# Kernel tuning notes

Hardware: AMD Instinct MI355X
Metric: run time of the kernel (lower is better)

## Reference

```python
import jax, jax.numpy as jnp
import numpy as np

LEAKY_SLOPE = 0.2  # PyG GATConv default negative_slope
EPS = 1e-16


def _gat_layer(h_in, src, dst, W, a_src, a_dst, b, concat):
    # h_in: [N, Fin]; src/dst: [Etot] (self-loops included); W: [Fin, H*C]
    N = h_in.shape[0]
    H, C = a_src.shape
    h = (h_in @ W).reshape(N, H, C)                       # [N,H,C]
    al_s = jnp.sum(h * a_src, axis=-1)                    # [N,H]
    al_d = jnp.sum(h * a_dst, axis=-1)                    # [N,H]
    e = jax.nn.leaky_relu(al_s[src] + al_d[dst], LEAKY_SLOPE)  # [E,H]
    emax = jax.ops.segment_max(e, dst, num_segments=N)    # segment softmax over dst
    p = jnp.exp(e - emax[dst])
    denom = jax.ops.segment_sum(p, dst, num_segments=N)
    alpha = p / (denom[dst] + EPS)                        # [E,H]
    out = jax.ops.segment_sum(h[src] * alpha[:, :, None], dst, num_segments=N)  # [N,H,C]
    out = out.reshape(N, H * C) if concat else out.mean(axis=1)
    return out + b


def setup_inputs() -> dict:
    key = jax.random.key(0)
    ks = jax.random.split(key, 16)
    N, E, Fin, Hd, Hh = 10000, 320000, 256, 128, 4

    def glorot(k, shape, fan_in):
        return jax.random.normal(k, shape, dtype=jnp.float32) * (1.0 / np.sqrt(fan_in))

    inp = {
        "x": jax.random.normal(ks[0], (N, Fin), dtype=jnp.float32),
        "edge_index": jax.random.randint(ks[1], (2, E), 0, N, dtype=jnp.int32),
        # conv1: Fin -> Hd x Hh heads, concat
        "W1": glorot(ks[2], (Fin, Hh * Hd), Fin),
        "a1_src": glorot(ks[3], (Hh, Hd), Hd),
        "a1_dst": glorot(ks[4], (Hh, Hd), Hd),
        "b1": jnp.zeros((Hh * Hd,), jnp.float32),
        # conv2: Hh*Hd -> Hd x Hh heads, concat
        "W2": glorot(ks[5], (Hh * Hd, Hh * Hd), Hh * Hd),
        "a2_src": glorot(ks[6], (Hh, Hd), Hd),
        "a2_dst": glorot(ks[7], (Hh, Hd), Hd),
        "b2": jnp.zeros((Hh * Hd,), jnp.float32),
        # conv3: Hh*Hd -> Hd, 1 head, concat=False (mean)
        "W3": glorot(ks[8], (Hh * Hd, Hd), Hh * Hd),
        "a3_src": glorot(ks[9], (1, Hd), Hd),
        "a3_dst": glorot(ks[10], (1, Hd), Hd),
        "b3": jnp.zeros((Hd,), jnp.float32),
        # classifier: Hd -> Hd//2 -> 2
        "Wc1": glorot(ks[11], (Hd, Hd // 2), Hd),
        "bc1": jnp.zeros((Hd // 2,), jnp.float32),
        "Wc2": glorot(ks[12], (Hd // 2, 2), Hd // 2),
        "bc2": jnp.zeros((2,), jnp.float32),
    }
    return inp


def reference(x, edge_index, W1, a1_src, a1_dst, b1, W2, a2_src, a2_dst, b2,
              W3, a3_src, a3_dst, b3, Wc1, bc1, Wc2, bc2):
    N = x.shape[0]
    loops = jnp.arange(N, dtype=edge_index.dtype)
    src = jnp.concatenate([edge_index[0], loops])  # PyG adds self-loops
    dst = jnp.concatenate([edge_index[1], loops])

    h = jax.nn.elu(_gat_layer(x, src, dst, W1, a1_src, a1_dst, b1, concat=True))
    h = jax.nn.elu(_gat_layer(h, src, dst, W2, a2_src, a2_dst, b2, concat=True))
    embeddings = _gat_layer(h, src, dst, W3, a3_src, a3_dst, b3, concat=False)  # [N, 128]
    out = jax.nn.relu(embeddings @ Wc1 + bc1) @ Wc2 + bc2  # [N, 2]
    return out, embeddings
```

## Files before the change

### kernel.cpp

```cpp
#include <hip/hip_runtime.h>
#include <cstddef>

#define LEAKY 0.2f
#define EPS_DEN 1e-16f

typedef short bf8_t __attribute__((ext_vector_type(8)));
typedef float f4_t __attribute__((ext_vector_type(4)));
typedef unsigned short us4_t __attribute__((ext_vector_type(4)));

__device__ __forceinline__ unsigned short f2bf(float f) {
    unsigned u = __float_as_uint(f);
    unsigned r = (u + 0x7fffu + ((u >> 16) & 1u)) >> 16;
    return (unsigned short)r;
}
__device__ __forceinline__ float bf2f(unsigned short h) {
    return __uint_as_float(((unsigned)h) << 16);
}

__global__ void hist_kernel(const int* __restrict__ dst, int* __restrict__ counts, int E) {
    int i = blockIdx.x * blockDim.x + threadIdx.x;
    if (i < E) atomicAdd(&counts[dst[i]], 1);
}

__global__ void scan1_kernel(int* __restrict__ cnt, int* __restrict__ bsum, int N) {
    __shared__ int s[256];
    int t = threadIdx.x;
    int i = blockIdx.x * 256 + t;
    int v = (i < N) ? cnt[i] : 0;
    s[t] = v;
    __syncthreads();
#pragma unroll
    for (int st = 1; st < 256; st <<= 1) {
        int add = (t >= st) ? s[t - st] : 0;
        __syncthreads();
        s[t] += add;
        __syncthreads();
    }
    if (i < N) cnt[i] = s[t] - v;
    if (t == 255) bsum[blockIdx.x] = s[255];
}

__global__ void scan3b_kernel(int* __restrict__ cnt, const int* __restrict__ bsum,
                              int* __restrict__ offs, int N, int NB) {
    __shared__ int sPre[64];
    __shared__ int sTot;
    int t = threadIdx.x;
    if (t < 64) {
        int v = (t < NB) ? bsum[t] : 0;
        int inc = v;
#pragma unroll
        for (int off = 1; off < 64; off <<= 1) {
            int u = __shfl_up(inc, off);
            if (t >= off) inc += u;
        }
        sPre[t] = inc - v;
        if (t == 63) sTot = inc;
    }
    __syncthreads();
    int i = blockIdx.x * 256 + t;
    if (i < N) {
        int o = cnt[i] + sPre[blockIdx.x];
        offs[i] = o;
        cnt[i] = o;
    }
    if (blockIdx.x == 0 && t == 0) offs[N] = sTot;
}

__global__ void scatter_kernel(const int* __restrict__ src, const int* __restrict__ dst,
                               int* __restrict__ cursor, int* __restrict__ csrc, int E) {
    int i = blockIdx.x * blockDim.x + threadIdx.x;
    if (i < E) {
        int d = dst[i];
        int pos = atomicAdd(&cursor[d], 1);
        csrc[pos] = src[i];
    }
}

__global__ void split_all_kernel(
    const float* __restrict__ x, unsigned short* __restrict__ xh, unsigned short* __restrict__ xl,
    int NBX,
    const float* __restrict__ W1, unsigned short* __restrict__ w1h, unsigned short* __restrict__ w1l,
    const float* __restrict__ W2, unsigned short* __restrict__ w2h, unsigned short* __restrict__ w2l,
    const float* __restrict__ W3, unsigned short* __restrict__ w3h, unsigned short* __restrict__ w3l) {
    int b = blockIdx.x, t = threadIdx.x;
    float v;
    unsigned short* ph;
    unsigned short* pl;
    int out;
    if (b < NBX) {
        int idx = b * 256 + t;
        v = x[idx];
        out = idx;
        ph = xh; pl = xl;
    } else if (b < NBX + 512) {
        int idx = (b - NBX) * 256 + t;
        v = W1[idx];
        int k = idx >> 9, n = idx & 511;
        out = n * 256 + k;
        ph = w1h; pl = w1l;
    } else if (b < NBX + 512 + 1024) {
        int idx = (b - NBX - 512) * 256 + t;
        v = W2[idx];
        int k = idx >> 9, n = idx & 511;
        out = n * 512 + k;
        ph = w2h; pl = w2l;
    } else {
        int idx = (b - NBX - 1536) * 256 + t;
        v = W3[idx];
        int k = idx >> 7, n = idx & 127;
        out = n * 512 + k;
        ph = w3h; pl = w3l;
    }
    unsigned short hv = f2bf(v);
    ph[out] = hv;
    pl[out] = f2bf(v - bf2f(hv));
}

__global__ __launch_bounds__(256) void mfma_gemm128_kernel(
    const unsigned short* __restrict__ Ahi, const unsigned short* __restrict__ Alo,
    const unsigned short* __restrict__ BThi, const unsigned short* __restrict__ BTlo,
    const float* __restrict__ a_src, const float* __restrict__ a_dst,
    float* __restrict__ C, float* __restrict__ als, float* __restrict__ ald,
    int M, int N, int K) {
    constexpr int BK = 64;
    __shared__ __align__(16) unsigned short sAh[128 * BK];
    __shared__ __align__(16) unsigned short sAl[128 * BK];
    __shared__ __align__(16) unsigned short sBh[128 * BK];
    __shared__ __align__(16) unsigned short sBl[128 * BK];
    __shared__ float sAls[128][2];
    __shared__ float sAld[128][2];
    int t = threadIdx.x;
    int w = t >> 6, lane = t & 63;
    int quad = lane >> 4, low = lane & 15;
    int m0 = blockIdx.y * 128, n0 = blockIdx.x * 128;
    int wm = (w & 1) * 64, wn = (w >> 1) * 64;

    f4_t acc[4][4];
#pragma unroll
    for (int i = 0; i < 4; i++)
#pragma unroll
        for (int j = 0; j < 4; j++) acc[i][j] = (f4_t){0.f, 0.f, 0.f, 0.f};

    int srow = lane >> 3;
    int schunk = lane & 7;

    for (int k0 = 0; k0 < K; k0 += BK) {
        __syncthreads();
#pragma unroll
        for (int inst = 0; inst < 4; inst++) {
            int rl = w * 32 + inst * 8 + srow;
            int gm = m0 + rl;
            if (gm >= M) gm = M - 1;
            size_t goff = (size_t)gm * K + k0 + schunk * 8;
            size_t loff = (size_t)rl * 128 - (size_t)(lane * 16) + (size_t)(srow * 128 + schunk * 16);
            loff = (size_t)(w * 32 + inst * 8) * 128;
            __builtin_amdgcn_global_load_lds(
                (const __attribute__((address_space(1))) void*)(Ahi + goff),
                (__attribute__((address_space(3))) void*)((char*)sAh + loff), 16, 0, 0);
            __builtin_amdgcn_global_load_lds(
                (const __attribute__((address_space(1))) void*)(Alo + goff),
                (__attribute__((address_space(3))) void*)((char*)sAl + loff), 16, 0, 0);
        }
#pragma unroll
        for (int inst = 0; inst < 4; inst++) {
            int rl = w * 32 + inst * 8 + srow;
            int gn = n0 + rl;
            size_t goff = (size_t)gn * K + k0 + schunk * 8;
            size_t loff = (size_t)(w * 32 + inst * 8) * 128;
            __builtin_amdgcn_global_load_lds(
                (const __attribute__((address_space(1))) void*)(BThi + goff),
                (__attribute__((address_space(3))) void*)((char*)sBh + loff), 16, 0, 0);
            __builtin_amdgcn_global_load_lds(
                (const __attribute__((address_space(1))) void*)(BTlo + goff),
                (__attribute__((address_space(3))) void*)((char*)sBl + loff), 16, 0, 0);
        }
        __syncthreads();

#pragma unroll
        for (int ks = 0; ks < 2; ks++) {
            int ko = ks * 32 + quad * 8;
            bf8_t afh[4], bfh[4], xx[4];
#pragma unroll
            for (int i = 0; i < 4; i++) {
                int row = wm + i * 16 + low;
                afh[i] = *(const bf8_t*)&sAh[row * BK + ko];
            }
#pragma unroll
            for (int j = 0; j < 4; j++) {
                int row = wn + j * 16 + low;
                bfh[j] = *(const bf8_t*)&sBh[row * BK + ko];
            }
#pragma unroll
            for (int i = 0; i < 4; i++)
#pragma unroll
                for (int j = 0; j < 4; j++)
                    acc[i][j] = __builtin_amdgcn_mfma_f32_16x16x32_bf16(afh[i], bfh[j], acc[i][j], 0, 0, 0);
#pragma unroll
            for (int j = 0; j < 4; j++) {
                int row = wn + j * 16 + low;
                xx[j] = *(const bf8_t*)&sBl[row * BK + ko];
            }
#pragma unroll
            for (int i = 0; i < 4; i++)
#pragma unroll
                for (int j = 0; j < 4; j++)
                    acc[i][j] = __builtin_amdgcn_mfma_f32_16x16x32_bf16(afh[i], xx[j], acc[i][j], 0, 0, 0);
#pragma unroll
            for (int i = 0; i < 4; i++) {
                int row = wm + i * 16 + low;
                xx[i] = *(const bf8_t*)&sAl[row * BK + ko];
            }
#pragma unroll
            for (int i = 0; i < 4; i++)
#pragma unroll
                for (int j = 0; j < 4; j++)
                    acc[i][j] = __builtin_amdgcn_mfma_f32_16x16x32_bf16(xx[i], bfh[j], acc[i][j], 0, 0, 0);
        }
    }

#pragma unroll
    for (int i = 0; i < 4; i++) {
#pragma unroll
        for (int r = 0; r < 4; r++) {
            int gm = m0 + wm + i * 16 + quad * 4 + r;
            if (gm >= M) continue;
#pragma unroll
            for (int j = 0; j < 4; j++) {
                int gn = n0 + wn + j * 16 + low;
                C[(size_t)gm * N + gn] = acc[i][j][r];
            }
        }
    }

    int hd = n0 >> 7;
    float as_[4], ad_[4];
#pragma unroll
    for (int j = 0; j < 4; j++) {
        int c = wn + j * 16 + low;
        as_[j] = a_src[hd * 128 + c];
        ad_[j] = a_dst[hd * 128 + c];
    }
    int chh = wn >> 6;
#pragma unroll
    for (int i = 0; i < 4; i++) {
#pragma unroll
        for (int r = 0; r < 4; r++) {
            float v = acc[i][0][r] * as_[0] + acc[i][1][r] * as_[1] +
                      acc[i][2][r] * as_[2] + acc[i][3][r] * as_[3];
            float vd = acc[i][0][r] * ad_[0] + acc[i][1][r] * ad_[1] +
                       acc[i][2][r] * ad_[2] + acc[i][3][r] * ad_[3];
#pragma unroll
            for (int off = 1; off < 16; off <<= 1) {
                v += __shfl_xor(v, off);
                vd += __shfl_xor(vd, off);
            }
            if (low == 0) {
                int row = wm + i * 16 + quad * 4 + r;
                sAls[row][chh] = v;
                sAld[row][chh] = vd;
            }
        }
    }
    __syncthreads();
    if (t < 128) {
        int gm = m0 + t;
        if (gm < M) {
            als[gm * 4 + hd] = sAls[t][0] + sAls[t][1];
            ald[gm * 4 + hd] = sAld[t][0] + sAld[t][1];
        }
    }
}

__global__ __launch_bounds__(256) void mfma_gemm64_kernel(
    const unsigned short* __restrict__ Ahi, const unsigned short* __restrict__ Alo,
    const unsigned short* __restrict__ BThi, const unsigned short* __restrict__ BTlo,
    const float* __restrict__ a_src, const float* __restrict__ a_dst,
    float* __restrict__ C, float* __restrict__ als, float* __restrict__ ald,
    int M, int N, int K) {
    constexpr int BK = 32;
    __shared__ __align__(16) unsigned short sAh[64 * BK];
    __shared__ __align__(16) unsigned short sAl[64 * BK];
    __shared__ __align__(16) unsigned short sBh[128 * BK];
    __shared__ __align__(16) unsigned short sBl[128 * BK];
    __shared__ float sAls[64][2];
    __shared__ float sAld[64][2];
    int t = threadIdx.x;
    int w = t >> 6, lane = t & 63;
    int quad = lane >> 4, low = lane & 15;
    int m0 = blockIdx.y * 64, n0 = blockIdx.x * 128;
    int wm = (w & 1) * 32, wn = (w >> 1) * 64;

    f4_t acc[2][4];
#pragma unroll
    for (int i = 0; i < 2; i++)
#pragma unroll
        for (int j = 0; j < 4; j++) acc[i][j] = (f4_t){0.f, 0.f, 0.f, 0.f};

    int srow = lane >> 2;
    int schunk = lane & 3;

    for (int k0 = 0; k0 < K; k0 += BK) {
        __syncthreads();
        {
            int gm = m0 + w * 16 + srow;
            if (gm >= M) gm = M - 1;
            size_t goff = (size_t)gm * K + k0 + schunk * 8;
            size_t loff = (size_t)(w * 1024);
            __builtin_amdgcn_global_load_lds(
                (const __attribute__((address_space(1))) void*)(Ahi + goff),
                (__attribute__((address_space(3))) void*)((char*)sAh + loff), 16, 0, 0);
            __builtin_amdgcn_global_load_lds(
                (const __attribute__((address_space(1))) void*)(Alo + goff),
                (__attribute__((address_space(3))) void*)((char*)sAl + loff), 16, 0, 0);
        }
#pragma unroll
        for (int inst = 0; inst < 2; inst++) {
            int gn = n0 + w * 32 + inst * 16 + srow;
            size_t goff = (size_t)gn * K + k0 + schunk * 8;
            size_t loff = (size_t)(w * 2048 + inst * 1024);
            __builtin_amdgcn_global_load_lds(
                (const __attribute__((address_space(1))) void*)(BThi + goff),
                (__attribute__((address_space(3))) void*)((char*)sBh + loff), 16, 0, 0);
            __builtin_amdgcn_global_load_lds(
                (const __attribute__((address_space(1))) void*)(BTlo + goff),
                (__attribute__((address_space(3))) void*)((char*)sBl + loff), 16, 0, 0);
        }
        __syncthreads();

        bf8_t afh[2], bfh[4], xx[4];
#pragma unroll
        for (int i = 0; i < 2; i++) {
            int row = wm + i * 16 + low;
            afh[i] = *(const bf8_t*)&sAh[row * BK + quad * 8];
        }
#pragma unroll
        for (int j = 0; j < 4; j++) {
            int row = wn + j * 16 + low;
            bfh[j] = *(const bf8_t*)&sBh[row * BK + quad * 8];
        }
#pragma unroll
        for (int i = 0; i < 2; i++)
#pragma unroll
            for (int j = 0; j < 4; j++)
                acc[i][j] = __builtin_amdgcn_mfma_f32_16x16x32_bf16(afh[i], bfh[j], acc[i][j], 0, 0, 0);
#pragma unroll
        for (int j = 0; j < 4; j++) {
            int row = wn + j * 16 + low;
            xx[j] = *(const bf8_t*)&sBl[row * BK + quad * 8];
        }
#pragma unroll
        for (int i = 0; i < 2; i++)
#pragma unroll
            for (int j = 0; j < 4; j++)
                acc[i][j] = __builtin_amdgcn_mfma_f32_16x16x32_bf16(afh[i], xx[j], acc[i][j], 0, 0, 0);
#pragma unroll
        for (int i = 0; i < 2; i++) {
            int row = wm + i * 16 + low;
            xx[i] = *(const bf8_t*)&sAl[row * BK + quad * 8];
        }
#pragma unroll
        for (int i = 0; i < 2; i++)
#pragma unroll
            for (int j = 0; j < 4; j++)
                acc[i][j] = __builtin_amdgcn_mfma_f32_16x16x32_bf16(xx[i], bfh[j], acc[i][j], 0, 0, 0);
    }

#pragma unroll
    for (int i = 0; i < 2; i++) {
#pragma unroll
        for (int r = 0; r < 4; r++) {
            int gm = m0 + wm + i * 16 + quad * 4 + r;
            if (gm >= M) continue;
#pragma unroll
            for (int j = 0; j < 4; j++) {
                int gn = n0 + wn + j * 16 + low;
                C[(size_t)gm * N + gn] = acc[i][j][r];
            }
        }
    }

    float as_[4], ad_[4];
#pragma unroll
    for (int j = 0; j < 4; j++) {
        int c = wn + j * 16 + low;
        as_[j] = a_src[c];
        ad_[j] = a_dst[c];
    }
    int chh = wn >> 6;
#pragma unroll
    for (int i = 0; i < 2; i++) {
#pragma unroll
        for (int r = 0; r < 4; r++) {
            float v = acc[i][0][r] * as_[0] + acc[i][1][r] * as_[1] +
                      acc[i][2][r] * as_[2] + acc[i][3][r] * as_[3];
            float vd = acc[i][0][r] * ad_[0] + acc[i][1][r] * ad_[1] +
                       acc[i][2][r] * ad_[2] + acc[i][3][r] * ad_[3];
#pragma unroll
            for (int off = 1; off < 16; off <<= 1) {
                v += __shfl_xor(v, off);
                vd += __shfl_xor(vd, off);
            }
            if (low == 0) {
                int row = wm + i * 16 + quad * 4 + r;
                sAls[row][chh] = v;
                sAld[row][chh] = vd;
            }
        }
    }
    __syncthreads();
    if (t < 64) {
        int gm = m0 + t;
        if (gm < M) {
            als[gm] = sAls[t][0] + sAls[t][1];
            ald[gm] = sAld[t][0] + sAld[t][1];
        }
    }
}

__global__ void stats_h4_kernel(const int* __restrict__ csrc, const int* __restrict__ offs,
                                const float* __restrict__ als, const float* __restrict__ ald,
                                float* __restrict__ pbuf, float* __restrict__ psf,
                                float* __restrict__ rden, int N, int E) {
    int wave = threadIdx.x >> 6, lane = threadIdx.x & 63;
    int n = blockIdx.x * 4 + wave;
    if (n >= N) return;
    int hd = lane & 3, es = lane >> 2;
    float aldn = ald[n * 4 + hd];
    float selfe = als[n * 4 + hd] + aldn;
    selfe = selfe > 0.f ? selfe : LEAKY * selfe;
    int beg = offs[n], end = offs[n + 1];
    int deg = end - beg;
    float* pb = pbuf + (size_t)hd * E;
    float m = selfe;
    float d = 0.f;
    if (deg <= 64) {
        float eR[4];
        int nch = (deg + 15) >> 4;
        for (int k = 0; k < nch; k++) {
            int idx = beg + k * 16 + es;
            float e = -1e30f;
            if (idx < end) {
                int s = csrc[idx];
                e = als[s * 4 + hd] + aldn;
                e = e > 0.f ? e : LEAKY * e;
                m = fmaxf(m, e);
            }
            eR[k] = e;
        }
#pragma unroll
        for (int off = 4; off < 64; off <<= 1) m = fmaxf(m, __shfl_xor(m, off));
        for (int k = 0; k < nch; k++) {
            int idx = beg + k * 16 + es;
            if (idx < end) {
                float p = __expf(eR[k] - m);
                pb[idx] = p;
                d += p;
            }
        }
    } else {
        for (int base = beg; base + es < end; base += 16) {
            int idx = base + es;
            int s = csrc[idx];
            float e = als[s * 4 + hd] + aldn;
            e = e > 0.f ? e : LEAKY * e;
            pb[idx] = e;
            m = fmaxf(m, e);
        }
#pragma unroll
        for (int off = 4; off < 64; off <<= 1) m = fmaxf(m, __shfl_xor(m, off));
        for (int base = beg; base + es < end; base += 16) {
            int idx = base + es;
            float p = __expf(pb[idx] - m);
            pb[idx] = p;
            d += p;
        }
    }
#pragma unroll
    for (int off = 4; off < 64; off <<= 1) d += __shfl_xor(d, off);
    float pself = __expf(selfe - m);
    float r = 1.0f / (d + pself + EPS_DEN);
    if (es == 0) {
        psf[n * 4 + hd] = pself;
        rden[n * 4 + hd] = r;
    }
}

template <bool DO_ELU>
__global__ __launch_bounds__(64) void gat_agg_hh_kernel(
    const float* __restrict__ h, const float* __restrict__ pbuf,
    const float* __restrict__ psf, const float* __restrict__ rden,
    const int* __restrict__ csrc, const int* __restrict__ offs,
    const float* __restrict__ bias, unsigned short* __restrict__ ohi,
    unsigned short* __restrict__ olo, int N, int E) {
    int gid = blockIdx.x;
    int hh = gid & 7;
    int n = gid >> 3;
    int head = hh >> 1;
    int lane = threadIdx.x;
    int eg = lane >> 4;
    int f0 = hh * 64 + (lane & 15) * 4;
    const float* pb = pbuf + (size_t)head * E;

    __shared__ int   sSrc[2][64];
    __shared__ float sP[2][64];
    int beg = offs[n], end = offs[n + 1];
    int nchunks = (end - beg + 63) >> 6;

    f4_t acc = (f4_t){0.f, 0.f, 0.f, 0.f};
    if (beg + lane < end) {
        sSrc[0][lane] = csrc[beg + lane] << 9;
        sP[0][lane] = pb[beg + lane];
    }
    for (int ch = 0; ch < nchunks; ch++) {
        int base = beg + ch * 64;
        int len = min(64, end - base);
        int buf = ch & 1;
        __syncthreads();
        int nbase = base + 64;
        if (ch + 1 < nchunks && nbase + lane < end) {
            sSrc[buf ^ 1][lane] = csrc[nbase + lane] << 9;
            sP[buf ^ 1][lane] = pb[nbase + lane];
        }
#pragma unroll 8
        for (int c = eg; c < len; c += 4) {
            const float* srow = h + (size_t)(unsigned)sSrc[buf][c] + f0;
            acc += sP[buf][c] * *(const f4_t*)srow;
        }
    }
    if (eg == 0) {
        f4_t x = *(const f4_t*)(h + (size_t)n * 512 + f0);
        acc += psf[n * 4 + head] * x;
    }
#pragma unroll
    for (int j = 0; j < 4; j++) {
        acc[j] += __shfl_xor(acc[j], 16);
        acc[j] += __shfl_xor(acc[j], 32);
    }
    if (lane < 16) {
        float r = rden[n * 4 + head];
        f4_t b = *(const f4_t*)(bias + f0);
        us4_t hs, ls;
#pragma unroll
        for (int j = 0; j < 4; j++) {
            float o = acc[j] * r + b[j];
            if (DO_ELU) o = o > 0.f ? o : (__expf(o) - 1.0f);
            unsigned short hv = f2bf(o);
            hs[j] = hv;
            ls[j] = f2bf(o - bf2f(hv));
        }
        size_t idx = (size_t)n * 512 + f0;
        *(us4_t*)&ohi[idx] = hs;
        *(us4_t*)&olo[idx] = ls;
    }
}

__global__ __launch_bounds__(256) void gat_agg_h1_cls_kernel(
    const float* __restrict__ h, const float* __restrict__ als,
    const float* __restrict__ ald, const int* __restrict__ csrc,
    const int* __restrict__ offs, const float* __restrict__ bias,
    const float* __restrict__ Wc1, const float* __restrict__ bc1,
    const float* __restrict__ Wc2, const float* __restrict__ bc2,
    float* __restrict__ emb, float* __restrict__ outp, int N) {
    int tid = threadIdx.x;
    int wave = tid >> 6;
    int n = blockIdx.x * 4 + wave;
    int lane = tid & 63;
    int eg = lane >> 4;
    int fl = (lane & 15) * 8;
    __shared__ float sW[128 * 64];
    __shared__ float semb[4][128];

    for (int i = tid; i < 128 * 64; i += 256) sW[i] = Wc1[i];

    int beg = offs[n], end = offs[n + 1];
    int deg = end - beg;
    float aldn = ald[n];
    float selfe = als[n] + aldn;
    selfe = selfe > 0.f ? selfe : LEAKY * selfe;

    f4_t a0 = (f4_t){0.f, 0.f, 0.f, 0.f};
    f4_t a1 = (f4_t){0.f, 0.f, 0.f, 0.f};
    float d = 0.f;
    float m;

    if (deg <= 64) {
        float e = -1e30f;
        int s = 0;
        if (lane < deg) {
            s = csrc[beg + lane];
            e = als[s] + aldn;
            e = e > 0.f ? e : LEAKY * e;
        }
        m = fmaxf(e, selfe);
#pragma unroll
        for (int off = 1; off < 64; off <<= 1) m = fmaxf(m, __shfl_xor(m, off));
        float p = (lane < deg) ? __expf(e - m) : 0.f;
        d = p;
        int sreg = s << 7;
        int maxit = (deg + 3) >> 2;
#pragma unroll 4
        for (int i = 0; i < maxit; i++) {
            int c = eg + i * 4;
            int soff = __shfl(sreg, c);
            float pc = __shfl(p, c);
            const float* srow = h + (size_t)(unsigned)soff + fl;
            a0 += pc * *(const f4_t*)(srow);
            a1 += pc * *(const f4_t*)(srow + 4);
        }
    } else {
        m = selfe;
        for (int i = beg + lane; i < end; i += 64) {
            int s = csrc[i];
            float e = als[s] + aldn;
            e = e > 0.f ? e : LEAKY * e;
            m = fmaxf(m, e);
        }
#pragma unroll
        for (int off = 1; off < 64; off <<= 1) m = fmaxf(m, __shfl_xor(m, off));
        for (int base = beg; base < end; base += 64) {
            int len = min(64, end - base);
            int sreg = 0;
            float p = 0.f;
            if (lane < len) {
                int s = csrc[base + lane];
                float e = als[s] + aldn;
                e = e > 0.f ? e : LEAKY * e;
                p = __expf(e - m);
                sreg = s << 7;
                d += p;
            }
            int maxit = (len + 3) >> 2;
#pragma unroll 4
            for (int i = 0; i < maxit; i++) {
                int c = eg + i * 4;
                int soff = __shfl(sreg, c);
                float pc = __shfl(p, c);
                const float* srow = h + (size_t)(unsigned)soff + fl;
                a0 += pc * *(const f4_t*)(srow);
                a1 += pc * *(const f4_t*)(srow + 4);
            }
        }
    }

    float pself = __expf(selfe - m);
    if (eg == 0) {
        const float* srow = h + (size_t)n * 128 + fl;
        a0 += pself * *(const f4_t*)(srow);
        a1 += pself * *(const f4_t*)(srow + 4);
    }
#pragma unroll
    for (int j = 0; j < 4; j++) {
        a0[j] += __shfl_xor(a0[j], 16);
        a0[j] += __shfl_xor(a0[j], 32);
        a1[j] += __shfl_xor(a1[j], 16);
        a1[j] += __shfl_xor(a1[j], 32);
    }
#pragma unroll
    for (int off = 1; off < 64; off <<= 1) d += __shfl_xor(d, off);
    float r = 1.0f / (d + pself + EPS_DEN);

    if (lane < 16) {
        int fo = lane * 8;
        f4_t b0 = *(const f4_t*)(bias + fo);
        f4_t b1 = *(const f4_t*)(bias + fo + 4);
        f4_t o0, o1;
#pragma unroll
        for (int j = 0; j < 4; j++) {
            o0[j] = a0[j] * r + b0[j];
            o1[j] = a1[j] * r + b1[j];
        }
        *(f4_t*)&semb[wave][fo] = o0;
        *(f4_t*)&semb[wave][fo + 4] = o1;
        *(f4_t*)&emb[(size_t)n * 128 + fo] = o0;
        *(f4_t*)&emb[(size_t)n * 128 + fo + 4] = o1;
    }
    __syncthreads();

    float cacc = bc1[lane];
#pragma unroll 8
    for (int k = 0; k < 128; k++) cacc += semb[wave][k] * sW[k * 64 + lane];
    cacc = fmaxf(cacc, 0.f);
    float o0 = cacc * Wc2[lane * 2 + 0];
    float o1 = cacc * Wc2[lane * 2 + 1];
#pragma unroll
    for (int off = 32; off; off >>= 1) {
        o0 += __shfl_down(o0, off);
        o1 += __shfl_down(o1, off);
    }
    if (lane == 0) {
        outp[n * 2 + 0] = o0 + bc2[0];
        outp[n * 2 + 1] = o1 + bc2[1];
    }
}

extern "C" void kernel_launch(void* const* d_in, const int* in_sizes, int n_in,
                              void* d_out, int out_size, void* d_ws, size_t ws_size,
                              hipStream_t stream) {
    const float* x      = (const float*)d_in[0];
    const int*   ei     = (const int*)d_in[1];
    const float* W1     = (const float*)d_in[2];
    const float* a1s    = (const float*)d_in[3];
    const float* a1d    = (const float*)d_in[4];
    const float* b1     = (const float*)d_in[5];
    const float* W2     = (const float*)d_in[6];
    const float* a2s    = (const float*)d_in[7];
    const float* a2d    = (const float*)d_in[8];
    const float* b2     = (const float*)d_in[9];
    const float* W3     = (const float*)d_in[10];
    const float* a3s    = (const float*)d_in[11];
    const float* a3d    = (const float*)d_in[12];
    const float* b3     = (const float*)d_in[13];
    const float* Wc1    = (const float*)d_in[14];
    const float* bc1    = (const float*)d_in[15];
    const float* Wc2    = (const float*)d_in[16];
    const float* bc2    = (const float*)d_in[17];

    const int N = in_sizes[0] / 256;
    const int E = in_sizes[1] / 2;
    const int F = 512;

    const int* src = ei;
    const int* dst = ei + E;

    auto align = [](size_t o) { return (o + 255) & ~(size_t)255; };
    size_t o = 0;
    size_t o_G     = o; o = align(o + (size_t)N * F * 4);
    size_t o_ahi   = o; o = align(o + (size_t)N * F * 2);
    size_t o_alo   = o; o = align(o + (size_t)N * F * 2);
    size_t o_xhi   = o; o = align(o + (size_t)N * 256 * 2);
    size_t o_xlo   = o; o = align(o + (size_t)N * 256 * 2);
    size_t o_w1h   = o; o = align(o + (size_t)512 * 256 * 2);
    size_t o_w1l   = o; o = align(o + (size_t)512 * 256 * 2);
    size_t o_w2h   = o; o = align(o + (size_t)512 * 512 * 2);
    size_t o_w2l   = o; o = align(o + (size_t)512 * 512 * 2);
    size_t o_w3h   = o; o = align(o + (size_t)128 * 512 * 2);
    size_t o_w3l   = o; o = align(o + (size_t)128 * 512 * 2);
    size_t o_als   = o; o = align(o + (size_t)N * 4 * 4);
    size_t o_ald   = o; o = align(o + (size_t)N * 4 * 4);
    size_t o_psf   = o; o = align(o + (size_t)N * 4 * 4);
    size_t o_rden  = o; o = align(o + (size_t)N * 4 * 4);
    size_t o_cnt   = o; o = align(o + (size_t)N * 4);
    size_t o_off   = o; o = align(o + (size_t)(N + 1) * 4);
    size_t o_bsum  = o; o = align(o + (size_t)64 * 4);
    size_t o_csrc  = o; o = align(o + (size_t)E * 4);
    size_t o_ebuf  = o; o = align(o + (size_t)E * 4 * 4);
    (void)ws_size;

    char* ws = (char*)d_ws;
    float* bufG  = (float*)(ws + o_G);
    unsigned short* act_hi = (unsigned short*)(ws + o_ahi);
    unsigned short* act_lo = (unsigned short*)(ws + o_alo);
    unsigned short* x_hi   = (unsigned short*)(ws + o_xhi);
    unsigned short* x_lo   = (unsigned short*)(ws + o_xlo);
    unsigned short* w1h = (unsigned short*)(ws + o_w1h);
    unsigned short* w1l = (unsigned short*)(ws + o_w1l);
    unsigned short* w2h = (unsigned short*)(ws + o_w2h);
    unsigned short* w2l = (unsigned short*)(ws + o_w2l);
    unsigned short* w3h = (unsigned short*)(ws + o_w3h);
    unsigned short* w3l = (unsigned short*)(ws + o_w3l);
    float* als  = (float*)(ws + o_als);
    float* ald  = (float*)(ws + o_ald);
    float* psf  = (float*)(ws + o_psf);
    float* rden = (float*)(ws + o_rden);
    int*   cnt  = (int*)(ws + o_cnt);
    int*   offs = (int*)(ws + o_off);
    int*   bsum = (int*)(ws + o_bsum);
    int*   csrc = (int*)(ws + o_csrc);
    float* ebuf = (float*)(ws + o_ebuf);

    float* outp = (float*)d_out;
    float* emb  = (float*)d_out + (size_t)N * 2;

    hipMemsetAsync(cnt, 0, (size_t)N * 4, stream);
    int eb = (E + 255) / 256;
    int nbs = (N + 255) / 256;
    hipLaunchKernelGGL(hist_kernel, dim3(eb), dim3(256), 0, stream, dst, cnt, E);
    hipLaunchKernelGGL(scan1_kernel, dim3(nbs), dim3(256), 0, stream, cnt, bsum, N);
    hipLaunchKernelGGL(scan3b_kernel, dim3(nbs), dim3(256), 0, stream, cnt, bsum, offs, N, nbs);
    hipLaunchKernelGGL(scatter_kernel, dim3(eb), dim3(256), 0, stream, src, dst, cnt, csrc, E);

    int NBX = N;
    hipLaunchKernelGGL(split_all_kernel, dim3(NBX + 512 + 1024 + 256), dim3(256), 0, stream,
                       x, x_hi, x_lo, NBX, W1, w1h, w1l, W2, w2h, w2l, W3, w3h, w3l);

    int nb4 = (N + 3) / 4;
    int gy128 = (N + 127) / 128;
    int gy64  = (N + 63) / 64;

    hipLaunchKernelGGL(mfma_gemm128_kernel, dim3(512 / 128, gy128), dim3(256), 0, stream,
                       x_hi, x_lo, w1h, w1l, a1s, a1d, bufG, als, ald, N, 512, 256);
    hipLaunchKernelGGL(stats_h4_kernel, dim3(nb4), dim3(256), 0, stream,
                       csrc, offs, als, ald, ebuf, psf, rden, N, E);
    hipLaunchKernelGGL((gat_agg_hh_kernel<true>), dim3(N * 8), dim3(64), 0, stream,
                       bufG, ebuf, psf, rden, csrc, offs, b1, act_hi, act_lo, N, E);

    hipLaunchKernelGGL(mfma_gemm128_kernel, dim3(512 / 128, gy128), dim3(256), 0, stream,
                       act_hi, act_lo, w2h, w2l, a2s, a2d, bufG, als, ald, N, 512, 512);
    hipLaunchKernelGGL(stats_h4_kernel, dim3(nb4), dim3(256), 0, stream,
                       csrc, offs, als, ald, ebuf, psf, rden, N, E);
    hipLaunchKernelGGL((gat_agg_hh_kernel<true>), dim3(N * 8), dim3(64), 0, stream,
                       bufG, ebuf, psf, rden, csrc, offs, b2, act_hi, act_lo, N, E);

    hipLaunchKernelGGL(mfma_gemm64_kernel, dim3(128 / 128, gy64), dim3(256), 0, stream,
                       act_hi, act_lo, w3h, w3l, a3s, a3d, bufG, als, ald, N, 128, 512);
    hipLaunchKernelGGL(gat_agg_h1_cls_kernel, dim3(nb4), dim3(256), 0, stream,
                       bufG, als, ald, csrc, offs, b3, Wc1, bc1, Wc2, bc2, emb, outp, N);
}
```

Baseline: 355.8 us.

## Pack source index with softmax weight and fuse histogram into split kernel

The stats kernel now writes an interleaved (pre-scaled source offset, probability) int2 per edge and head, so the aggregation kernel reads one 8-byte record instead of separate csrc and probability arrays. The aggregation kernel's shared-memory double buffering is replaced by a single buffer with two barriers per chunk. The degree histogram is folded into the bf16 split kernel to save one launch. The edge buffer doubles in size, which adds write traffic in the stats pass, and the removed prefetch may expose load latency.

Measured after the change: 355.9 us. No clear change (+0.0%).

```diff
diff --git a/kernel.cpp b/kernel.cpp
--- a/kernel.cpp
+++ b/kernel.cpp
@@ -15,11 +15,6 @@
 }
 __device__ __forceinline__ float bf2f(unsigned short h) {
     return __uint_as_float(((unsigned)h) << 16);
-}
-
-__global__ void hist_kernel(const int* __restrict__ dst, int* __restrict__ counts, int E) {
-    int i = blockIdx.x * blockDim.x + threadIdx.x;
-    if (i < E) atomicAdd(&counts[dst[i]], 1);
 }
 
 __global__ void scan1_kernel(int* __restrict__ cnt, int* __restrict__ bsum, int N) {
@@ -76,13 +71,20 @@
     }
 }
 
-__global__ void split_all_kernel(
+__global__ void hist_split_kernel(
+    const int* __restrict__ dst, int* __restrict__ counts, int E, int EB,
     const float* __restrict__ x, unsigned short* __restrict__ xh, unsigned short* __restrict__ xl,
     int NBX,
     const float* __restrict__ W1, unsigned short* __restrict__ w1h, unsigned short* __restrict__ w1l,
     const float* __restrict__ W2, unsigned short* __restrict__ w2h, unsigned short* __restrict__ w2l,
     const float* __restrict__ W3, unsigned short* __restrict__ w3h, unsigned short* __restrict__ w3l) {
     int b = blockIdx.x, t = threadIdx.x;
+    if (b < EB) {
+        int i = b * 256 + t;
+        if (i < E) atomicAdd(&counts[dst[i]], 1);
+        return;
+    }
+    b -= EB;
     float v;
     unsigned short* ph;
     unsigned short* pl;
@@ -152,8 +154,7 @@
             int gm = m0 + rl;
             if (gm >= M) gm = M - 1;
             size_t goff = (size_t)gm * K + k0 + schunk * 8;
-            size_t loff = (size_t)rl * 128 - (size_t)(lane * 16) + (size_t)(srow * 128 + schunk * 16);
-            loff = (size_t)(w * 32 + inst * 8) * 128;
+            size_t loff = (size_t)(w * 32 + inst * 8) * 128;
             __builtin_amdgcn_global_load_lds(
                 (const __attribute__((address_space(1))) void*)(Ahi + goff),
                 (__attribute__((address_space(3))) void*)((char*)sAh + loff), 16, 0, 0);
@@ -419,7 +420,7 @@
 
 __global__ void stats_h4_kernel(const int* __restrict__ csrc, const int* __restrict__ offs,
                                 const float* __restrict__ als, const float* __restrict__ ald,
-                                float* __restrict__ pbuf, float* __restrict__ psf,
+                                int2* __restrict__ pbuf2, float* __restrict__ psf,
                                 float* __restrict__ rden, int N, int E) {
     int wave = threadIdx.x >> 6, lane = threadIdx.x & 63;
     int n = blockIdx.x * 4 + wave;
@@ -430,22 +431,25 @@
     selfe = selfe > 0.f ? selfe : LEAKY * selfe;
     int beg = offs[n], end = offs[n + 1];
     int deg = end - beg;
-    float* pb = pbuf + (size_t)hd * E;
+    int2* pb = pbuf2 + (size_t)hd * E;
     float m = selfe;
     float d = 0.f;
     if (deg <= 64) {
         float eR[4];
+        int sR[4];
         int nch = (deg + 15) >> 4;
         for (int k = 0; k < nch; k++) {
             int idx = beg + k * 16 + es;
             float e = -1e30f;
+            int s = 0;
             if (idx < end) {
-                int s = csrc[idx];
+                s = csrc[idx];
                 e = als[s * 4 + hd] + aldn;
                 e = e > 0.f ? e : LEAKY * e;
                 m = fmaxf(m, e);
             }
             eR[k] = e;
+            sR[k] = s;
         }
 #pragma unroll
         for (int off = 4; off < 64; off <<= 1) m = fmaxf(m, __shfl_xor(m, off));
@@ -453,7 +457,7 @@
             int idx = beg + k * 16 + es;
             if (idx < end) {
                 float p = __expf(eR[k] - m);
-                pb[idx] = p;
+                pb[idx] = make_int2(sR[k] << 9, __float_as_int(p));
                 d += p;
             }
         }
@@ -463,15 +467,16 @@
             int s = csrc[idx];
             float e = als[s * 4 + hd] + aldn;
             e = e > 0.f ? e : LEAKY * e;
-            pb[idx] = e;
+            pb[idx] = make_int2(s << 9, __float_as_int(e));
             m = fmaxf(m, e);
         }
 #pragma unroll
         for (int off = 4; off < 64; off <<= 1) m = fmaxf(m, __shfl_xor(m, off));
         for (int base = beg; base + es < end; base += 16) {
             int idx = base + es;
-            float p = __expf(pb[idx] - m);
-            pb[idx] = p;
+            int2 se = pb[idx];
+            float p = __expf(__int_as_float(se.y) - m);
+            pb[idx] = make_int2(se.x, __float_as_int(p));
             d += p;
         }
     }
@@ -487,11 +492,11 @@
 
 template <bool DO_ELU>
 __global__ __launch_bounds__(64) void gat_agg_hh_kernel(
-    const float* __restrict__ h, const float* __restrict__ pbuf,
+    const float* __restrict__ h, const int2* __restrict__ pbuf2,
     const float* __restrict__ psf, const float* __restrict__ rden,
-    const int* __restrict__ csrc, const int* __restrict__ offs,
-    const float* __restrict__ bias, unsigned short* __restrict__ ohi,
-    unsigned short* __restrict__ olo, int N, int E) {
+    const int* __restrict__ offs, const float* __restrict__ bias,
+    unsigned short* __restrict__ ohi, unsigned short* __restrict__ olo,
+    int N, int E) {
     int gid = blockIdx.x;
     int hh = gid & 7;
     int n = gid >> 3;
@@ -499,32 +504,22 @@
     int lane = threadIdx.x;
     int eg = lane >> 4;
     int f0 = hh * 64 + (lane & 15) * 4;
-    const float* pb = pbuf + (size_t)head * E;
-
-    __shared__ int   sSrc[2][64];
-    __shared__ float sP[2][64];
+    const int2* pb = pbuf2 + (size_t)head * E;
+
+    __shared__ __align__(8) int2 sE[64];
     int beg = offs[n], end = offs[n + 1];
-    int nchunks = (end - beg + 63) >> 6;
 
     f4_t acc = (f4_t){0.f, 0.f, 0.f, 0.f};
-    if (beg + lane < end) {
-        sSrc[0][lane] = csrc[beg + lane] << 9;
-        sP[0][lane] = pb[beg + lane];
-    }
-    for (int ch = 0; ch < nchunks; ch++) {
-        int base = beg + ch * 64;
+    for (int base = beg; base < end; base += 64) {
         int len = min(64, end - base);
-        int buf = ch & 1;
         __syncthreads();
-        int nbase = base + 64;
-        if (ch + 1 < nchunks && nbase + lane < end) {
-            sSrc[buf ^ 1][lane] = csrc[nbase + lane] << 9;
-            sP[buf ^ 1][lane] = pb[nbase + lane];
-        }
+        if (lane < len) sE[lane] = pb[base + lane];
+        __syncthreads();
 #pragma unroll 8
         for (int c = eg; c < len; c += 4) {
-            const float* srow = h + (size_t)(unsigned)sSrc[buf][c] + f0;
-            acc += sP[buf][c] * *(const f4_t*)srow;
+            int2 se = sE[c];
+            const float* srow = h + (size_t)(unsigned)se.x + f0;
+            acc += __int_as_float(se.y) * *(const f4_t*)srow;
         }
     }
     if (eg == 0) {
@@ -743,7 +738,7 @@
     size_t o_off   = o; o = align(o + (size_t)(N + 1) * 4);
     size_t o_bsum  = o; o = align(o + (size_t)64 * 4);
     size_t o_csrc  = o; o = align(o + (size_t)E * 4);
-    size_t o_ebuf  = o; o = align(o + (size_t)E * 4 * 4);
+    size_t o_ebuf  = o; o = align(o + (size_t)E * 4 * 8);
     (void)ws_size;
 
     char* ws = (char*)d_ws;
@@ -766,23 +761,23 @@
     int*   offs = (int*)(ws + o_off);
     int*   bsum = (int*)(ws + o_bsum);
     int*   csrc = (int*)(ws + o_csrc);
-    float* ebuf = (float*)(ws + o_ebuf);
+    int2*  ebuf2 = (int2*)(ws + o_ebuf);
 
     float* outp = (float*)d_out;
     float* emb  = (float*)d_out + (size_t)N * 2;
 
     hipMemsetAsync(cnt, 0, (size_t)N * 4, stream);
     int eb = (E + 255) / 256;
+    int NBX = N;
+    hipLaunchKernelGGL(hist_split_kernel, dim3(eb + NBX + 512 + 1024 + 256), dim3(256), 0, stream,
+                       dst, cnt, E, eb,
+                       x, x_hi, x_lo, NBX, W1, w1h, w1l, W2, w2h, w2l, W3, w3h, w3l);
+
     int nbs = (N + 255) / 256;
-    hipLaunchKernelGGL(hist_kernel, dim3(eb), dim3(256), 0, stream, dst, cnt, E);
     hipLaunchKernelGGL(scan1_kernel, dim3(nbs), dim3(256), 0, stream, cnt, bsum, N);
     hipLaunchKernelGGL(scan3b_kernel, dim3(nbs), dim3(256), 0, stream, cnt, bsum, offs, N, nbs);
     hipLaunchKernelGGL(scatter_kernel, dim3(eb), dim3(256), 0, stream, src, dst, cnt, csrc, E);
 
-    int NBX = N;
-    hipLaunchKernelGGL(split_all_kernel, dim3(NBX + 512 + 1024 + 256), dim3(256), 0, stream,
-                       x, x_hi, x_lo, NBX, W1, w1h, w1l, W2, w2h, w2l, W3, w3h, w3l);
-
     int nb4 = (N + 3) / 4;
     int gy128 = (N + 127) / 128;
     int gy64  = (N + 63) / 64;
@@ -790,16 +785,16 @@
     hipLaunchKernelGGL(mfma_gemm128_kernel, dim3(512 / 128, gy128), dim3(256), 0, stream,
                        x_hi, x_lo, w1h, w1l, a1s, a1d, bufG, als, ald, N, 512, 256);
     hipLaunchKernelGGL(stats_h4_kernel, dim3(nb4), dim3(256), 0, stream,
-                       csrc, offs, als, ald, ebuf, psf, rden, N, E);
+                       csrc, offs, als, ald, ebuf2, psf, rden, N, E);
     hipLaunchKernelGGL((gat_agg_hh_kernel<true>), dim3(N * 8), dim3(64), 0, stream,
-                       bufG, ebuf, psf, rden, csrc, offs, b1, act_hi, act_lo, N, E);
+                       bufG, ebuf2, psf, rden, offs, b1, act_hi, act_lo, N, E);
 
     hipLaunchKernelGGL(mfma_gemm128_kernel, dim3(512 / 128, gy128), dim3(256), 0, stream,
                        act_hi, act_lo, w2h, w2l, a2s, a2d, bufG, als, ald, N, 512, 512);
     hipLaunchKernelGGL(stats_h4_kernel, dim3(nb4), dim3(256), 0, stream,
-                       csrc, offs, als, ald, ebuf, psf, rden, N, E);
+                       csrc, offs, als, ald, ebuf2, psf, rden, N, E);
     hipLaunchKernelGGL((gat_agg_hh_kernel<true>), dim3(N * 8), dim3(64), 0, stream,
-                       bufG, ebuf, psf, rden, csrc, offs, b2, act_hi, act_lo, N, E);
+                       bufG, ebuf2, psf, rden, offs, b2, act_hi, act_lo, N, E);
 
     hipLaunchKernelGGL(mfma_gemm64_kernel, dim3(128 / 128, gy64), dim3(256), 0, stream,
                        act_hi, act_lo, w3h, w3l, a3s, a3d, bufG, als, ald, N, 128, 512);
```
